# Kernel optimization log

Measured on AMD Instinct MI355X. Metric: run time of the kernel, lower is better.

## Reference

```python
import jax, jax.numpy as jnp
import numpy as np

KW = 3          # kernel_width
PAD = (KW - 1) // 2


def setup_inputs() -> dict:
    key = jax.random.key(0)
    ks = jax.random.split(key, 7)
    B, Lq, Lk, D, C = 8, 1024, 1024, 512, 512  # D=q_size, C=k_size
    return {
        "q": jax.random.normal(ks[0], (B, Lq, D), jnp.float32),
        "k": jax.random.normal(ks[1], (B, Lk, C), jnp.float32),
        "W_kernel": jax.random.normal(ks[2], (D, C * KW), jnp.float32) * (1.0 / np.sqrt(D)),
        "b_kernel": jax.random.normal(ks[3], (C * KW,), jnp.float32) * 0.02,
        "W_bias": jax.random.normal(ks[4], (D, 1), jnp.float32) * (1.0 / np.sqrt(D)),
        "b_bias": jax.random.normal(ks[5], (1,), jnp.float32) * 0.02,
        "bias_b": jax.random.normal(ks[6], (1,), jnp.float32),
    }


def reference(q, k, W_kernel, b_kernel, W_bias, b_bias, bias_b):
    B, Lq, D = q.shape
    _, Lk, C = k.shape
    # per-(batch, query) dynamic conv kernels: [B, Lq, C, KW]
    kernel = (q @ W_kernel + b_kernel).reshape(B, Lq, C, KW)
    # per-(batch, query) scalar bias: [B, Lq]
    bias = (q @ W_bias + b_bias)[..., 0]
    # windowed view of k (cross-correlation with 'same' padding)
    kpad = jnp.pad(k, ((0, 0), (PAD, PAD), (0, 0)))  # [B, Lk+2*PAD, C]
    win_idx = jnp.arange(Lk)[:, None] + jnp.arange(KW)[None, :]  # [Lk, KW]
    kwin = kpad[:, win_idx, :]  # [B, Lk, KW, C]
    # a[b,i,j] = sum_{c,w} kernel[b,i,c,w] * kpad[b, j+w, c] + bias[b,i] + bias_b
    a_ij = jnp.einsum('bicw,bjwc->bij', kernel, kwin)
    return a_ij + bias[:, :, None] + bias_b
```

## Files before the change

kernel.cpp:

```cpp
#include <hip/hip_runtime.h>


typedef __attribute__((ext_vector_type(8))) short s8vec;
typedef __attribute__((ext_vector_type(4))) float floatx4;

__device__ __forceinline__ unsigned short f2bf(float f) {
    union { float f; unsigned u; } v; v.f = f;
    unsigned r = (v.u + 0x7FFFu + ((v.u >> 16) & 1u)) >> 16;
    return (unsigned short)r;
}

__device__ __forceinline__ void gl2lds16(const void* g, void* l) {
    __builtin_amdgcn_global_load_lds(
        (__attribute__((address_space(1))) void*)(g),
        (__attribute__((address_space(3))) void*)(l), 16, 0, 0);
}

__global__ void cvt_all(const float* __restrict__ q, const float* __restrict__ k,
                        unsigned short* __restrict__ qbf, unsigned short* __restrict__ kp,
                        const float* __restrict__ W, unsigned short* __restrict__ Wt2,
                        const float* __restrict__ b_kernel, float* __restrict__ tj) {
    __shared__ float ldsw[1536];
    int blk = blockIdx.x;
    if (blk < 4104) {
        int t = blk * 256 + threadIdx.x;
        if (t < 524288) {
            const float4* p = (const float4*)q + 2 * (size_t)t;
            float4 a = p[0], b = p[1];
            union { unsigned short s[8]; uint4 v; } o;
            o.s[0]=f2bf(a.x); o.s[1]=f2bf(a.y); o.s[2]=f2bf(a.z); o.s[3]=f2bf(a.w);
            o.s[4]=f2bf(b.x); o.s[5]=f2bf(b.y); o.s[6]=f2bf(b.z); o.s[7]=f2bf(b.w);
            ((uint4*)qbf)[t] = o.v;
        } else if (t < 1048576) {
            int e8 = t - 524288;
            size_t e = (size_t)e8 * 8;
            int b = e8 >> 16;
            int j = (e8 >> 6) & 1023;
            int c = (e8 & 63) * 8;
            const float4* p = (const float4*)(k + e);
            float4 a = p[0], bb = p[1];
            union { unsigned short s[8]; uint4 v; } o;
            o.s[0]=f2bf(a.x); o.s[1]=f2bf(a.y); o.s[2]=f2bf(a.z); o.s[3]=f2bf(a.w);
            o.s[4]=f2bf(bb.x); o.s[5]=f2bf(bb.y); o.s[6]=f2bf(bb.z); o.s[7]=f2bf(bb.w);
            *(uint4*)(kp + ((size_t)(b * 1028 + j + 1) * 512 + c)) = o.v;
        } else if (t < 1050624) {
            int z = t - 1048576;
            int b = z >> 8, r = (z >> 6) & 3, ch = z & 63;
            int row = r ? (1024 + r) : 0;
            *(uint4*)(kp + ((size_t)(b * 1028 + row) * 512 + ch * 8)) = make_uint4(0u,0u,0u,0u);
        }
    } else if (blk < 4616) {
        int d = blk - 4104;
        const float4* wrow = (const float4*)(W + (size_t)d * 1536);
        for (int e = threadIdx.x; e < 384; e += 256) {
            float4 v = wrow[e];
            float va[4] = { v.x, v.y, v.z, v.w };
            #pragma unroll
            for (int i = 0; i < 4; i++) {
                int idx = e * 4 + i;
                int c = idx / 3, w = idx - c * 3;
                ldsw[w * 512 + c] = va[i];
            }
        }
        __syncthreads();
        for (int p = threadIdx.x; p < 192; p += 256) {
            union { unsigned short s[8]; uint4 v; } o;
            #pragma unroll
            for (int i = 0; i < 8; i++) o.s[i] = f2bf(ldsw[p * 8 + i]);
            *(uint4*)(Wt2 + (size_t)d * 1536 + p * 8) = o.v;
        }
    } else {
        int p = blk - 4616;
        int b = p >> 5, j0r = (p & 31) * 32;
        for (int e = threadIdx.x; e < 1536; e += 256) {
            float v = b_kernel[e];
            int c = e / 3, w = e - c * 3;
            ldsw[w * 512 + c] = v;
        }
        __syncthreads();
        int wave = threadIdx.x >> 6, lane = threadIdx.x & 63;
        float bw[3][8];
        #pragma unroll
        for (int w = 0; w < 3; w++)
            #pragma unroll
            for (int i = 0; i < 8; i++) bw[w][i] = ldsw[w * 512 + lane * 8 + i];
        const float* kb = k + (size_t)b * 1024 * 512;
        #pragma unroll
        for (int rr = 0; rr < 8; rr++) {
            int j = j0r + wave * 8 + rr;
            float s = 0.0f;
            #pragma unroll
            for (int w = 0; w < 3; w++) {
                int src = j + w - 1;
                if (src >= 0 && src < 1024) {
                    const float4* kr = (const float4*)(kb + (size_t)src * 512) + lane * 2;
                    float4 a0 = kr[0], a1 = kr[1];
                    s += a0.x*bw[w][0] + a0.y*bw[w][1] + a0.z*bw[w][2] + a0.w*bw[w][3]
                       + a1.x*bw[w][4] + a1.y*bw[w][5] + a1.z*bw[w][6] + a1.w*bw[w][7];
                }
            }
            #pragma unroll
            for (int off = 32; off > 0; off >>= 1) s += __shfl_down(s, off);
            if (lane == 0) tj[b * 1024 + j] = s;
        }
    }
}

__global__ __launch_bounds__(256) void gemm_V(const unsigned short* __restrict__ kp,
                                              const unsigned short* __restrict__ Wt2,
                                              const float* __restrict__ Wbias,
                                              unsigned short* __restrict__ V) {
    __shared__ unsigned short lds_a[2][128 * 64];
    __shared__ unsigned short lds_b[2][64 * 64];
    int g = blockIdx.x;
    int b = g & 7, slot = g >> 3;
    int j0 = (slot >> 3) * 128;
    int n0 = (slot & 7) * 64;
    int tid = threadIdx.x, wid = tid >> 6, lane = tid & 63;
    int wm = wid >> 1, wn = wid & 1;
    int crow = lane >> 3;
    int scol = ((lane & 7) ^ crow) * 8;
    const unsigned short* kpb = kp + (size_t)(b * 1028 + j0) * 512;
    floatx4 acc[4][2] = {};

    auto STAGE = [&](int buf, int kk) {
        #pragma unroll
        for (int s = 0; s < 6; ++s) {
            int t = wid * 6 + s;
            if (t < 16) {
                const unsigned short* ga = kpb + (size_t)(t * 8 + crow) * 512 + kk + scol;
                gl2lds16(ga, (char*)lds_a[buf] + t * 1024);
            } else {
                int u = t - 16;
                const unsigned short* gb = Wt2 + (size_t)(n0 + u * 8 + crow) * 1536 + kk + scol;
                gl2lds16(gb, (char*)lds_b[buf] + u * 1024);
            }
        }
    };

    STAGE(0, 0);
    __syncthreads();
    int cur = 0;
    int ra = lane & 15, hi = lane >> 4;
    for (int kt = 0; kt < 24; ++kt) {
        if (kt < 23) STAGE(cur ^ 1, (kt + 1) * 64);
        #pragma unroll
        for (int ks = 0; ks < 2; ++ks) {
            s8vec af[4], bfr[2];
            #pragma unroll
            for (int mi = 0; mi < 4; mi++) {
                int R = wm * 64 + mi * 16 + ra;
                af[mi] = *(const s8vec*)((const char*)lds_a[cur] + R * 128 + (((ks << 2) + hi) ^ (R & 7)) * 16);
            }
            #pragma unroll
            for (int ni = 0; ni < 2; ni++) {
                int R = wn * 32 + ni * 16 + ra;
                bfr[ni] = *(const s8vec*)((const char*)lds_b[cur] + R * 128 + (((ks << 2) + hi) ^ (R & 7)) * 16);
            }
            #pragma unroll
            for (int mi = 0; mi < 4; mi++)
                #pragma unroll
                for (int ni = 0; ni < 2; ni++)
                    acc[mi][ni] = __builtin_amdgcn_mfma_f32_16x16x32_bf16(af[mi], bfr[ni], acc[mi][ni], 0, 0, 0);
        }
        if (kt < 23) { __syncthreads(); cur ^= 1; }
    }

    int cl = lane & 15, qd = lane >> 4;
    #pragma unroll
    for (int mi = 0; mi < 4; mi++) {
        #pragma unroll
        for (int ni = 0; ni < 2; ni++) {
            int col = n0 + wn * 32 + ni * 16 + cl;
            float wb = Wbias[col];
            #pragma unroll
            for (int r = 0; r < 4; r++) {
                int m_g = b * 1024 + j0 + wm * 64 + mi * 16 + qd * 4 + r;
                V[(size_t)m_g * 512 + col] = f2bf(acc[mi][ni][r] + wb);
            }
        }
    }
}

__global__ __launch_bounds__(256) void gemm_QV(const unsigned short* __restrict__ qbf,
                                               const unsigned short* __restrict__ V,
                                               const float* __restrict__ tj,
                                               const float* __restrict__ b_bias,
                                               const float* __restrict__ bias_b,
                                               float* __restrict__ out) {
    __shared__ unsigned short lds_a[2][128 * 64];
    __shared__ unsigned short lds_b[2][128 * 64];
    int g = blockIdx.x;
    int b = g & 7, slot = g >> 3;
    int i0 = (slot >> 3) * 128;
    int j0 = (slot & 7) * 128;
    int tid = threadIdx.x, wid = tid >> 6, lane = tid & 63;
    int wm = wid >> 1, wn = wid & 1;
    int crow = lane >> 3;
    int scol = ((lane & 7) ^ crow) * 8;
    const unsigned short* Ab = qbf + (size_t)b * 1024 * 512;
    const unsigned short* Bb = V + (size_t)b * 1024 * 512;
    floatx4 acc[4][4] = {};

    auto STAGE = [&](int buf, int kk) {
        #pragma unroll
        for (int s = 0; s < 8; ++s) {
            int t = wid * 8 + s;
            if (t < 16) {
                const unsigned short* ga = Ab + (size_t)(i0 + t * 8 + crow) * 512 + kk + scol;
                gl2lds16(ga, (char*)lds_a[buf] + t * 1024);
            } else {
                int u = t - 16;
                const unsigned short* gb = Bb + (size_t)(j0 + u * 8 + crow) * 512 + kk + scol;
                gl2lds16(gb, (char*)lds_b[buf] + u * 1024);
            }
        }
    };

    STAGE(0, 0);
    __syncthreads();
    int cur = 0;
    int ra = lane & 15, hi = lane >> 4;
    for (int kt = 0; kt < 8; ++kt) {
        if (kt < 7) STAGE(cur ^ 1, (kt + 1) * 64);
        #pragma unroll
        for (int ks = 0; ks < 2; ++ks) {
            s8vec af[4], bfr[4];
            #pragma unroll
            for (int mi = 0; mi < 4; mi++) {
                int R = wm * 64 + mi * 16 + ra;
                af[mi] = *(const s8vec*)((const char*)lds_a[cur] + R * 128 + (((ks << 2) + hi) ^ (R & 7)) * 16);
            }
            #pragma unroll
            for (int ni = 0; ni < 4; ni++) {
                int R = wn * 64 + ni * 16 + ra;
                bfr[ni] = *(const s8vec*)((const char*)lds_b[cur] + R * 128 + (((ks << 2) + hi) ^ (R & 7)) * 16);
            }
            #pragma unroll
            for (int mi = 0; mi < 4; mi++)
                #pragma unroll
                for (int ni = 0; ni < 4; ni++)
                    acc[mi][ni] = __builtin_amdgcn_mfma_f32_16x16x32_bf16(af[mi], bfr[ni], acc[mi][ni], 0, 0, 0);
        }
        if (kt < 7) { __syncthreads(); cur ^= 1; }
    }

    int cl = lane & 15, qd = lane >> 4;
    float bbsum = b_bias[0] + bias_b[0];
    float tv[4];
    #pragma unroll
    for (int ni = 0; ni < 4; ni++) {
        int j_loc = wn * 64 + ni * 16 + cl;
        tv[ni] = tj[b * 1024 + j0 + j_loc] + bbsum;
    }
    #pragma unroll
    for (int mi = 0; mi < 4; mi++) {
        #pragma unroll
        for (int r = 0; r < 4; r++) {
            int i_g = i0 + wm * 64 + mi * 16 + qd * 4 + r;
            float* orow = out + ((size_t)(b * 1024 + i_g)) * 1024 + j0;
            #pragma unroll
            for (int ni = 0; ni < 4; ni++) {
                int j_loc = wn * 64 + ni * 16 + cl;
                orow[j_loc] = acc[mi][ni][r] + tv[ni];
            }
        }
    }
}

extern "C" void kernel_launch(void* const* d_in, const int* in_sizes, int n_in,
                              void* d_out, int out_size, void* d_ws, size_t ws_size,
                              hipStream_t stream) {
    const float* q        = (const float*)d_in[0];
    const float* k        = (const float*)d_in[1];
    const float* W_kernel = (const float*)d_in[2];
    const float* b_kernel = (const float*)d_in[3];
    const float* W_bias   = (const float*)d_in[4];
    const float* b_bias   = (const float*)d_in[5];
    const float* bias_b   = (const float*)d_in[6];
    float* out = (float*)d_out;

    char* ws = (char*)d_ws;
    unsigned short* q_bf = (unsigned short*)(ws);
    unsigned short* kp   = (unsigned short*)(ws + 8388608);
    unsigned short* Wt2  = (unsigned short*)(ws + 8388608 + 8421376 + 16384);
    unsigned short* V    = (unsigned short*)(ws + 8388608 + 8421376 + 16384 + 1572864);
    float*          tj   = (float*)(ws + 8388608 + 8421376 + 16384 + 1572864 + 8388608);

    cvt_all<<<4872, 256, 0, stream>>>(q, k, q_bf, kp, W_kernel, Wt2, b_kernel, tj);
    gemm_V<<<512, 256, 0, stream>>>(kp, Wt2, W_bias, V);
    gemm_QV<<<512, 256, 0, stream>>>(q_bf, V, tj, b_bias, bias_b, out);
}
```

Baseline: 133.4 us.

## Reuse staged k tile across the three window offsets in gemm_V

The kernel previously treated the windowed k as an im2col-style K dimension, reloading the A tile for each 64-wide chunk of K=1536. It now stages a 136-row k tile once per channel chunk and reuses it for all three window shifts by offsetting the row index, while only the W tile changes each step. This cuts global-to-LDS traffic for A by roughly a factor of three, at the cost of a slightly larger LDS buffer and a row-shifted read pattern that may change swizzle bank behaviour.

New measurement: 138.1 us. 1.03x slower.

```diff
diff --git a/kernel.cpp b/kernel.cpp
--- a/kernel.cpp
+++ b/kernel.cpp
@@ -110,7 +110,7 @@
                                               const unsigned short* __restrict__ Wt2,
                                               const float* __restrict__ Wbias,
                                               unsigned short* __restrict__ V) {
-    __shared__ unsigned short lds_a[2][128 * 64];
+    __shared__ unsigned short lds_a[2][136 * 64];
     __shared__ unsigned short lds_b[2][64 * 64];
     int g = blockIdx.x;
     int b = g & 7, slot = g >> 3;
@@ -123,39 +123,51 @@
     const unsigned short* kpb = kp + (size_t)(b * 1028 + j0) * 512;
     floatx4 acc[4][2] = {};
 
-    auto STAGE = [&](int buf, int kk) {
-        #pragma unroll
-        for (int s = 0; s < 6; ++s) {
-            int t = wid * 6 + s;
-            if (t < 16) {
-                const unsigned short* ga = kpb + (size_t)(t * 8 + crow) * 512 + kk + scol;
+    auto STAGE_A = [&](int buf, int c0) {
+        #pragma unroll
+        for (int s = 0; s < 5; ++s) {
+            int t = wid * 5 + s;
+            if (t < 17) {
+                const unsigned short* ga = kpb + (size_t)(t * 8 + crow) * 512 + c0 + scol;
                 gl2lds16(ga, (char*)lds_a[buf] + t * 1024);
-            } else {
-                int u = t - 16;
-                const unsigned short* gb = Wt2 + (size_t)(n0 + u * 8 + crow) * 1536 + kk + scol;
-                gl2lds16(gb, (char*)lds_b[buf] + u * 1024);
             }
         }
     };
-
-    STAGE(0, 0);
+    auto STAGE_B = [&](int buf, int w, int c0) {
+        #pragma unroll
+        for (int s = 0; s < 2; ++s) {
+            int t = wid * 2 + s;
+            const unsigned short* gb = Wt2 + (size_t)(n0 + t * 8 + crow) * 1536
+                                           + w * 512 + c0 + scol;
+            gl2lds16(gb, (char*)lds_b[buf] + t * 1024);
+        }
+    };
+
+    STAGE_A(0, 0);
+    STAGE_B(0, 0, 0);
     __syncthreads();
-    int cur = 0;
+    int curA = 0, curB = 0;
     int ra = lane & 15, hi = lane >> 4;
-    for (int kt = 0; kt < 24; ++kt) {
-        if (kt < 23) STAGE(cur ^ 1, (kt + 1) * 64);
+    for (int s = 0; s < 24; ++s) {
+        int c8 = s / 3, w = s - c8 * 3;
+        if (s + 1 < 24) {
+            int s1 = s + 1, c81 = s1 / 3, w1 = s1 - c81 * 3;
+            STAGE_B(curB ^ 1, w1, c81 * 64);
+        }
+        if (w == 0 && c8 + 1 < 8)
+            STAGE_A(curA ^ 1, (c8 + 1) * 64);
         #pragma unroll
         for (int ks = 0; ks < 2; ++ks) {
             s8vec af[4], bfr[2];
             #pragma unroll
             for (int mi = 0; mi < 4; mi++) {
-                int R = wm * 64 + mi * 16 + ra;
-                af[mi] = *(const s8vec*)((const char*)lds_a[cur] + R * 128 + (((ks << 2) + hi) ^ (R & 7)) * 16);
+                int R = wm * 64 + mi * 16 + ra + w;
+                af[mi] = *(const s8vec*)((const char*)lds_a[curA] + R * 128 + (((ks << 2) + hi) ^ (R & 7)) * 16);
             }
             #pragma unroll
             for (int ni = 0; ni < 2; ni++) {
                 int R = wn * 32 + ni * 16 + ra;
-                bfr[ni] = *(const s8vec*)((const char*)lds_b[cur] + R * 128 + (((ks << 2) + hi) ^ (R & 7)) * 16);
+                bfr[ni] = *(const s8vec*)((const char*)lds_b[curB] + R * 128 + (((ks << 2) + hi) ^ (R & 7)) * 16);
             }
             #pragma unroll
             for (int mi = 0; mi < 4; mi++)
@@ -163,7 +175,11 @@
                 for (int ni = 0; ni < 2; ni++)
                     acc[mi][ni] = __builtin_amdgcn_mfma_f32_16x16x32_bf16(af[mi], bfr[ni], acc[mi][ni], 0, 0, 0);
         }
-        if (kt < 23) { __syncthreads(); cur ^= 1; }
+        if (s < 23) {
+            __syncthreads();
+            curB ^= 1;
+            if (w == 2) curA ^= 1;
+        }
     }
 
     int cl = lane & 15, qd = lane >> 4;
```

## Fuse k bf16 conversion with per-row bias dot products into one pass

Applied to the files above, without the earlier changes.

The k-to-bf16 conversion and the b_kernel bias term computation are merged so each k row is read from global memory once. Instead of re-reading three shifted rows per output, each row computes three partial dot products (one per tap) into a padded buffer. The final gemm then sums the three shifted partials when adding the bias. This removes the roughly threefold re-read of k in the bias path, at the cost of three reductions per row and three loads in the epilogue.

New measurement: 127.4 us. -4.5%, faster.

```diff
diff --git a/kernel.cpp b/kernel.cpp
--- a/kernel.cpp
+++ b/kernel.cpp
@@ -19,38 +19,63 @@
 __global__ void cvt_all(const float* __restrict__ q, const float* __restrict__ k,
                         unsigned short* __restrict__ qbf, unsigned short* __restrict__ kp,
                         const float* __restrict__ W, unsigned short* __restrict__ Wt2,
-                        const float* __restrict__ b_kernel, float* __restrict__ tj) {
+                        const float* __restrict__ b_kernel, float* __restrict__ spart) {
     __shared__ float ldsw[1536];
     int blk = blockIdx.x;
-    if (blk < 4104) {
+    if (blk < 2048) {
         int t = blk * 256 + threadIdx.x;
-        if (t < 524288) {
-            const float4* p = (const float4*)q + 2 * (size_t)t;
-            float4 a = p[0], b = p[1];
+        const float4* p = (const float4*)q + 2 * (size_t)t;
+        float4 a = p[0], b = p[1];
+        union { unsigned short s[8]; uint4 v; } o;
+        o.s[0]=f2bf(a.x); o.s[1]=f2bf(a.y); o.s[2]=f2bf(a.z); o.s[3]=f2bf(a.w);
+        o.s[4]=f2bf(b.x); o.s[5]=f2bf(b.y); o.s[6]=f2bf(b.z); o.s[7]=f2bf(b.w);
+        ((uint4*)qbf)[t] = o.v;
+    } else if (blk < 3072) {
+        int p = blk - 2048;
+        int b = p >> 7;
+        for (int e = threadIdx.x; e < 1536; e += 256) {
+            float v = b_kernel[e];
+            int c = e / 3, w = e - c * 3;
+            ldsw[w * 512 + c] = v;
+        }
+        __syncthreads();
+        int wave = threadIdx.x >> 6, lane = threadIdx.x & 63;
+        float bw[3][8];
+        #pragma unroll
+        for (int w = 0; w < 3; w++)
+            #pragma unroll
+            for (int i = 0; i < 8; i++) bw[w][i] = ldsw[w * 512 + lane * 8 + i];
+        const float* kb = k + (size_t)b * 1024 * 512;
+        #pragma unroll
+        for (int rr = 0; rr < 2; rr++) {
+            int j = (p & 127) * 8 + wave * 2 + rr;
+            const float4* kr = (const float4*)(kb + (size_t)j * 512) + lane * 2;
+            float4 a0 = kr[0], a1 = kr[1];
             union { unsigned short s[8]; uint4 v; } o;
-            o.s[0]=f2bf(a.x); o.s[1]=f2bf(a.y); o.s[2]=f2bf(a.z); o.s[3]=f2bf(a.w);
-            o.s[4]=f2bf(b.x); o.s[5]=f2bf(b.y); o.s[6]=f2bf(b.z); o.s[7]=f2bf(b.w);
-            ((uint4*)qbf)[t] = o.v;
-        } else if (t < 1048576) {
-            int e8 = t - 524288;
-            size_t e = (size_t)e8 * 8;
-            int b = e8 >> 16;
-            int j = (e8 >> 6) & 1023;
-            int c = (e8 & 63) * 8;
-            const float4* p = (const float4*)(k + e);
-            float4 a = p[0], bb = p[1];
-            union { unsigned short s[8]; uint4 v; } o;
-            o.s[0]=f2bf(a.x); o.s[1]=f2bf(a.y); o.s[2]=f2bf(a.z); o.s[3]=f2bf(a.w);
-            o.s[4]=f2bf(bb.x); o.s[5]=f2bf(bb.y); o.s[6]=f2bf(bb.z); o.s[7]=f2bf(bb.w);
-            *(uint4*)(kp + ((size_t)(b * 1028 + j + 1) * 512 + c)) = o.v;
-        } else if (t < 1050624) {
-            int z = t - 1048576;
-            int b = z >> 8, r = (z >> 6) & 3, ch = z & 63;
-            int row = r ? (1024 + r) : 0;
-            *(uint4*)(kp + ((size_t)(b * 1028 + row) * 512 + ch * 8)) = make_uint4(0u,0u,0u,0u);
-        }
-    } else if (blk < 4616) {
-        int d = blk - 4104;
+            o.s[0]=f2bf(a0.x); o.s[1]=f2bf(a0.y); o.s[2]=f2bf(a0.z); o.s[3]=f2bf(a0.w);
+            o.s[4]=f2bf(a1.x); o.s[5]=f2bf(a1.y); o.s[6]=f2bf(a1.z); o.s[7]=f2bf(a1.w);
+            *(uint4*)(kp + ((size_t)(b * 1028 + j + 1) * 512 + lane * 8)) = o.v;
+            float s0 = a0.x*bw[0][0] + a0.y*bw[0][1] + a0.z*bw[0][2] + a0.w*bw[0][3]
+                     + a1.x*bw[0][4] + a1.y*bw[0][5] + a1.z*bw[0][6] + a1.w*bw[0][7];
+            float s1 = a0.x*bw[1][0] + a0.y*bw[1][1] + a0.z*bw[1][2] + a0.w*bw[1][3]
+                     + a1.x*bw[1][4] + a1.y*bw[1][5] + a1.z*bw[1][6] + a1.w*bw[1][7];
+            float s2 = a0.x*bw[2][0] + a0.y*bw[2][1] + a0.z*bw[2][2] + a0.w*bw[2][3]
+                     + a1.x*bw[2][4] + a1.y*bw[2][5] + a1.z*bw[2][6] + a1.w*bw[2][7];
+            #pragma unroll
+            for (int off = 32; off > 0; off >>= 1) {
+                s0 += __shfl_down(s0, off);
+                s1 += __shfl_down(s1, off);
+                s2 += __shfl_down(s2, off);
+            }
+            if (lane == 0) {
+                float* sb = spart + b * 1028 + j + 1;
+                sb[0]     = s0;
+                sb[8224]  = s1;
+                sb[16448] = s2;
+            }
+        }
+    } else if (blk < 3584) {
+        int d = blk - 3072;
         const float4* wrow = (const float4*)(W + (size_t)d * 1536);
         for (int e = threadIdx.x; e < 384; e += 256) {
             float4 v = wrow[e];
@@ -69,39 +94,17 @@
             for (int i = 0; i < 8; i++) o.s[i] = f2bf(ldsw[p * 8 + i]);
             *(uint4*)(Wt2 + (size_t)d * 1536 + p * 8) = o.v;
         }
+    } else if (blk < 3592) {
+        int z = (blk - 3584) * 256 + threadIdx.x;
+        int b = z >> 8, r = (z >> 6) & 3, ch = z & 63;
+        int row = r ? (1024 + r) : 0;
+        *(uint4*)(kp + ((size_t)(b * 1028 + row) * 512 + ch * 8)) = make_uint4(0u,0u,0u,0u);
     } else {
-        int p = blk - 4616;
-        int b = p >> 5, j0r = (p & 31) * 32;
-        for (int e = threadIdx.x; e < 1536; e += 256) {
-            float v = b_kernel[e];
-            int c = e / 3, w = e - c * 3;
-            ldsw[w * 512 + c] = v;
-        }
-        __syncthreads();
-        int wave = threadIdx.x >> 6, lane = threadIdx.x & 63;
-        float bw[3][8];
-        #pragma unroll
-        for (int w = 0; w < 3; w++)
-            #pragma unroll
-            for (int i = 0; i < 8; i++) bw[w][i] = ldsw[w * 512 + lane * 8 + i];
-        const float* kb = k + (size_t)b * 1024 * 512;
-        #pragma unroll
-        for (int rr = 0; rr < 8; rr++) {
-            int j = j0r + wave * 8 + rr;
-            float s = 0.0f;
-            #pragma unroll
-            for (int w = 0; w < 3; w++) {
-                int src = j + w - 1;
-                if (src >= 0 && src < 1024) {
-                    const float4* kr = (const float4*)(kb + (size_t)src * 512) + lane * 2;
-                    float4 a0 = kr[0], a1 = kr[1];
-                    s += a0.x*bw[w][0] + a0.y*bw[w][1] + a0.z*bw[w][2] + a0.w*bw[w][3]
-                       + a1.x*bw[w][4] + a1.y*bw[w][5] + a1.z*bw[w][6] + a1.w*bw[w][7];
-                }
-            }
-            #pragma unroll
-            for (int off = 32; off > 0; off >>= 1) s += __shfl_down(s, off);
-            if (lane == 0) tj[b * 1024 + j] = s;
+        int t = threadIdx.x;
+        if (t < 48) {
+            int w = t >> 4, rem = t & 15;
+            int b = rem >> 1, pos = (rem & 1) ? 1025 : 0;
+            spart[w * 8224 + b * 1028 + pos] = 0.0f;
         }
     }
 }
@@ -184,7 +187,7 @@
 
 __global__ __launch_bounds__(256) void gemm_QV(const unsigned short* __restrict__ qbf,
                                                const unsigned short* __restrict__ V,
-                                               const float* __restrict__ tj,
+                                               const float* __restrict__ spart,
                                                const float* __restrict__ b_bias,
                                                const float* __restrict__ bias_b,
                                                float* __restrict__ out) {
@@ -247,11 +250,12 @@
 
     int cl = lane & 15, qd = lane >> 4;
     float bbsum = b_bias[0] + bias_b[0];
+    const float* sb = spart + b * 1028;
     float tv[4];
     #pragma unroll
     for (int ni = 0; ni < 4; ni++) {
-        int j_loc = wn * 64 + ni * 16 + cl;
-        tv[ni] = tj[b * 1024 + j0 + j_loc] + bbsum;
+        int jg = j0 + wn * 64 + ni * 16 + cl;
+        tv[ni] = sb[jg] + sb[8224 + jg + 1] + sb[16448 + jg + 2] + bbsum;
     }
     #pragma unroll
     for (int mi = 0; mi < 4; mi++) {
@@ -285,9 +289,9 @@
     unsigned short* kp   = (unsigned short*)(ws + 8388608);
     unsigned short* Wt2  = (unsigned short*)(ws + 8388608 + 8421376 + 16384);
     unsigned short* V    = (unsigned short*)(ws + 8388608 + 8421376 + 16384 + 1572864);
-    float*          tj   = (float*)(ws + 8388608 + 8421376 + 16384 + 1572864 + 8388608);
-
-    cvt_all<<<4872, 256, 0, stream>>>(q, k, q_bf, kp, W_kernel, Wt2, b_kernel, tj);
+    float*          sp   = (float*)(ws + 8388608 + 8421376 + 16384 + 1572864 + 8388608);
+
+    cvt_all<<<3593, 256, 0, stream>>>(q, k, q_bf, kp, W_kernel, Wt2, b_kernel, sp);
     gemm_V<<<512, 256, 0, stream>>>(kp, Wt2, W_bias, V);
-    gemm_QV<<<512, 256, 0, stream>>>(q_bf, V, tj, b_bias, bias_b, out);
-}
+    gemm_QV<<<512, 256, 0, stream>>>(q_bf, V, sp, b_bias, bias_b, out);
+}
```
